# Kernel tuning notes

Hardware: AMD Instinct MI355X
Metric: run time of the kernel (lower is better)

The kernel has to match this reference:

```python
import jax, jax.numpy as jnp
import numpy as np
import math

D, DF, H, L, V, T_MAX = 768, 3072, 12, 4, 32000, 2048
HD = D // H
B, T = 2, 2048


def setup_inputs() -> dict:
    key = jax.random.key(0)
    ks = jax.random.split(key, 20)
    s = 0.02
    inp = {
        'ids': jax.random.randint(ks[0], (B, T), 0, V),
        'te': jax.random.normal(ks[1], (V, D), jnp.float32) * s,  # tied with head
        'pe': jax.random.normal(ks[2], (T_MAX, D), jnp.float32) * s,
        'ln1_s': jnp.ones((L, D), jnp.float32),
        'ln1_b': jnp.zeros((L, D), jnp.float32),
        'qkv_w': jax.random.normal(ks[3], (L, D, 3 * H * HD), jnp.float32) * s,
        'qkv_b': jnp.zeros((L, 3 * H * HD), jnp.float32),
        'out_w': jax.random.normal(ks[4], (L, H * HD, D), jnp.float32) * s,
        'out_b': jnp.zeros((L, D), jnp.float32),
        'ln2_s': jnp.ones((L, D), jnp.float32),
        'ln2_b': jnp.zeros((L, D), jnp.float32),
        'up_w': jax.random.normal(ks[5], (L, D, DF), jnp.float32) * s,
        'up_b': jnp.zeros((L, DF), jnp.float32),
        'dn_w': jax.random.normal(ks[6], (L, DF, D), jnp.float32) * s,
        'dn_b': jnp.zeros((L, D), jnp.float32),
        'lnf_s': jnp.ones((D,), jnp.float32),
        'lnf_b': jnp.zeros((D,), jnp.float32),
    }
    return inp


def _layernorm(x, s, b, eps=1e-5):
    mu = jnp.mean(x, axis=-1, keepdims=True)
    var = jnp.mean(jnp.square(x - mu), axis=-1, keepdims=True)
    return (x - mu) * jax.lax.rsqrt(var + eps) * s + b


def reference(ids, te, pe, ln1_s, ln1_b, qkv_w, qkv_b, out_w, out_b,
              ln2_s, ln2_b, up_w, up_b, dn_w, dn_b, lnf_s, lnf_b):
    b, t = ids.shape
    x = te[ids] + pe[jnp.arange(t)][None, :, :]  # [b,t,d]
    causal = jnp.tril(jnp.ones((t, t), bool))[None, None]  # [1,1,t,t]
    neg = jnp.asarray(-jnp.inf, x.dtype)
    for i in range(L):
        h = _layernorm(x, ln1_s[i], ln1_b[i])
        qkv = (h @ qkv_w[i] + qkv_b[i]).reshape(b, t, 3, H, HD)
        q, k, v = [jnp.moveaxis(qkv[:, :, j], 1, 2) for j in range(3)]  # [b,h,t,hd]
        sc = jnp.einsum('bhqd,bhkd->bhqk', q, k) / math.sqrt(HD)
        sc = jnp.where(causal, sc, neg)
        a = jax.nn.softmax(sc, axis=-1)
        o = jnp.einsum('bhqk,bhkd->bhqd', a, v)
        o = jnp.moveaxis(o, 1, 2).reshape(b, t, H * HD)
        x = x + o @ out_w[i] + out_b[i]
        h = _layernorm(x, ln2_s[i], ln2_b[i])
        x = x + jax.nn.silu(h @ up_w[i] + up_b[i]) @ dn_w[i] + dn_b[i]
    logits = _layernorm(x, lnf_s, lnf_b) @ te.T  # tied head, no bias
    return logits
```

## Files before the change

kernel.cpp:

```cpp
#include <hip/hip_runtime.h>

typedef unsigned short u16;

#define TSEQ 2048
#define DMODEL 768
#define DFF 3072
#define NHEAD 12
#define HDIM 64
#define NLAYER 4
#define NVOCAB 32000
#define MROWS 4096

typedef __attribute__((ext_vector_type(8))) __bf16 bf16x8;
typedef __attribute__((ext_vector_type(4))) float f32x4;
typedef __attribute__((ext_vector_type(8))) unsigned short us8;

__device__ __forceinline__ float u2f(u16 u) {
  return __uint_as_float(((unsigned int)u) << 16);
}
__device__ __forceinline__ u16 f2bu(float f) {
  unsigned int u = __float_as_uint(f);
  u += 0x7fffu + ((u >> 16) & 1u);
  return (u16)(u >> 16);
}
__device__ __forceinline__ int probe_f32(const void* probe) {
  return ((const u16*)probe)[0] == 0 ? 1 : 0;
}
__device__ __forceinline__ float ldf(const void* p, size_t i, int f32) {
  return f32 ? ((const float*)p)[i] : u2f(((const u16*)p)[i]);
}
__device__ __forceinline__ void ld8(const void* p, size_t i, int f32, float* o) {
  if (f32) {
    const float* q = (const float*)p + i;
    float4 a = *(const float4*)q, b = *(const float4*)(q + 4);
    o[0]=a.x; o[1]=a.y; o[2]=a.z; o[3]=a.w; o[4]=b.x; o[5]=b.y; o[6]=b.z; o[7]=b.w;
  } else {
    const u16* q = (const u16*)p + i;
    ushort4 a = *(const ushort4*)q, b = *(const ushort4*)(q + 4);
    o[0]=u2f(a.x); o[1]=u2f(a.y); o[2]=u2f(a.z); o[3]=u2f(a.w);
    o[4]=u2f(b.x); o[5]=u2f(b.y); o[6]=u2f(b.z); o[7]=u2f(b.w);
  }
}
__device__ __forceinline__ us8 pack8(const float* f) {
  us8 r;
#pragma unroll
  for (int i = 0; i < 8; i++) r[i] = f2bu(f[i]);
  return r;
}

__global__ __launch_bounds__(256) void embed_kernel(const int* __restrict__ ids,
    const void* __restrict__ te, const void* __restrict__ pe, float* __restrict__ x,
    const void* probe) {
  int f32 = probe_f32(probe);
  int m = blockIdx.x;
  int t = m & (TSEQ - 1);
  int id = ids[m];
  float* xr = x + (size_t)m * DMODEL;
  for (int d = threadIdx.x; d < DMODEL; d += 256)
    xr[d] = ldf(te, (size_t)id * DMODEL + d, f32) + ldf(pe, (size_t)t * DMODEL + d, f32);
}

__global__ __launch_bounds__(256) void ln_kernel(const float* __restrict__ x,
    const void* __restrict__ s, const void* __restrict__ b, long soff,
    float* __restrict__ h, const void* probe) {
  int f32 = probe_f32(probe);
  int m = blockIdx.x;
  const float* xr = x + (size_t)m * DMODEL;
  float v[3];
  float lsum = 0.f, lsq = 0.f;
#pragma unroll
  for (int j = 0; j < 3; j++) {
    float t = xr[threadIdx.x + j * 256];
    v[j] = t; lsum += t; lsq += t * t;
  }
#pragma unroll
  for (int off = 32; off > 0; off >>= 1) {
    lsum += __shfl_down(lsum, off);
    lsq  += __shfl_down(lsq, off);
  }
  __shared__ float wsum[4], wsq[4];
  __shared__ float mu_s, rs_s;
  int wid = threadIdx.x >> 6, lane = threadIdx.x & 63;
  if (lane == 0) { wsum[wid] = lsum; wsq[wid] = lsq; }
  __syncthreads();
  if (threadIdx.x == 0) {
    float su = wsum[0] + wsum[1] + wsum[2] + wsum[3];
    float sq = wsq[0] + wsq[1] + wsq[2] + wsq[3];
    float mu = su * (1.f / DMODEL);
    float var = sq * (1.f / DMODEL) - mu * mu;
    mu_s = mu;
    rs_s = rsqrtf(var + 1e-5f);
  }
  __syncthreads();
  float mu = mu_s, rs = rs_s;
  float* hr = h + (size_t)m * DMODEL;
#pragma unroll
  for (int j = 0; j < 3; j++) {
    int d = threadIdx.x + j * 256;
    hr[d] = (v[j] - mu) * rs * ldf(s, soff + d, f32) + ldf(b, soff + d, f32);
  }
}

__global__ __launch_bounds__(256) void wtrans_kernel(const void* __restrict__ W,
    u16* __restrict__ Wt, int K, int N, const void* probe) {
  const int f32 = probe_f32(probe);
  __shared__ u16 t[64][33];
  const size_t ls = (size_t)K * N;
  const size_t off = (size_t)blockIdx.z * ls;
  const int k0 = blockIdx.y << 6, n0 = blockIdx.x << 5;
  const int tid = threadIdx.x;
  const int tn = tid & 31, tk8 = tid >> 5;
#pragma unroll
  for (int p = 0; p < 8; p++) {
    int k = (p << 3) + tk8;
    t[k][tn] = f2bu(ldf(W, off + (size_t)(k0 + k) * N + n0 + tn, f32));
  }
  __syncthreads();
  const int kp = (tid & 31) << 1, nb = tid >> 5;
#pragma unroll
  for (int p = 0; p < 4; p++) {
    int n = (p << 3) + nb;
    ushort2 v; v.x = t[kp][n]; v.y = t[kp + 1][n];
    *(ushort2*)&Wt[off + (size_t)(n0 + n) * K + k0 + kp] = v;
  }
}

__global__ __launch_bounds__(256) void cvt_bf16_kernel(const void* __restrict__ src,
    u16* __restrict__ dst, size_t n, const void* probe) {
  const int f32 = probe_f32(probe);
  size_t i = ((size_t)blockIdx.x * 256 + threadIdx.x) * 8;
  if (i >= n) return;
  float v[8];
  ld8(src, i, f32, v);
  *(us8*)&dst[i] = pack8(v);
}

__global__ __launch_bounds__(256) void gemm_nn(const float* __restrict__ A,
    const void* __restrict__ W, long woff, const void* __restrict__ bias, long boff,
    const float* resid, float* C, int N, int K, int mode, const void* probe) {
  int f32 = probe_f32(probe);
  __shared__ float As[16][132];
  __shared__ float Bs[16][132];
  const int tid = threadIdx.x;
  const int m0 = blockIdx.y << 7, n0 = blockIdx.x << 7;
  const int rbase = (tid >> 4) << 3;
  const int cbase = (tid & 15) << 3;
  const int ar = tid >> 1, ak = (tid & 1) << 3;
  const int wk = tid >> 4, wc = (tid & 15) << 3;
  float acc[8][8];
#pragma unroll
  for (int i = 0; i < 8; i++)
#pragma unroll
    for (int j = 0; j < 8; j++) acc[i][j] = 0.f;

  const float* Ab = A + (size_t)(m0 + ar) * K + ak;
  for (int k0 = 0; k0 < K; k0 += 16) {
    float4 a0 = *(const float4*)(Ab + k0);
    float4 a1 = *(const float4*)(Ab + k0 + 4);
    As[ak + 0][ar] = a0.x; As[ak + 1][ar] = a0.y; As[ak + 2][ar] = a0.z; As[ak + 3][ar] = a0.w;
    As[ak + 4][ar] = a1.x; As[ak + 5][ar] = a1.y; As[ak + 6][ar] = a1.z; As[ak + 7][ar] = a1.w;
    float w[8];
    ld8(W, (size_t)woff + (size_t)(k0 + wk) * N + n0 + wc, f32, w);
    *(float4*)&Bs[wk][wc]     = make_float4(w[0], w[1], w[2], w[3]);
    *(float4*)&Bs[wk][wc + 4] = make_float4(w[4], w[5], w[6], w[7]);
    __syncthreads();
#pragma unroll
    for (int kk = 0; kk < 16; kk++) {
      float a[8], b[8];
      *(float4*)&a[0] = *(const float4*)&As[kk][rbase];
      *(float4*)&a[4] = *(const float4*)&As[kk][rbase + 4];
      *(float4*)&b[0] = *(const float4*)&Bs[kk][cbase];
      *(float4*)&b[4] = *(const float4*)&Bs[kk][cbase + 4];
#pragma unroll
      for (int i = 0; i < 8; i++)
#pragma unroll
        for (int j = 0; j < 8; j++)
          acc[i][j] = fmaf(a[i], b[j], acc[i][j]);
    }
    __syncthreads();
  }
  float bv[8];
#pragma unroll
  for (int j = 0; j < 8; j++) bv[j] = ldf(bias, boff + n0 + cbase + j, f32);
#pragma unroll
  for (int i = 0; i < 8; i++) {
    size_t off = (size_t)(m0 + rbase + i) * N + n0 + cbase;
    float v[8];
#pragma unroll
    for (int j = 0; j < 8; j++) v[j] = acc[i][j] + bv[j];
    if (mode == 1) {
      float4 r0 = *(const float4*)(resid + off);
      float4 r1 = *(const float4*)(resid + off + 4);
      v[0] += r0.x; v[1] += r0.y; v[2] += r0.z; v[3] += r0.w;
      v[4] += r1.x; v[5] += r1.y; v[6] += r1.z; v[7] += r1.w;
    } else if (mode == 2) {
#pragma unroll
      for (int j = 0; j < 8; j++) v[j] = v[j] / (1.f + __expf(-v[j]));
    }
    *(float4*)(C + off)     = make_float4(v[0], v[1], v[2], v[3]);
    *(float4*)(C + off + 4) = make_float4(v[4], v[5], v[6], v[7]);
  }
}

__global__ __launch_bounds__(256) void gemm_mfma(const float* __restrict__ A,
    const u16* __restrict__ Wt, long woff, const void* __restrict__ bias, long boff,
    const float* resid, float* C, int N, int K, int mode, const void* probe) {
  const int f32 = probe_f32(probe);
  __shared__ __align__(16) u16 As[128][40];
  __shared__ __align__(16) u16 Bs[128][40];
  const int tid = threadIdx.x;
  const int m0 = blockIdx.y << 7, n0 = blockIdx.x << 7;
  const int lane = tid & 63;
  const int wr = ((tid >> 7) & 1) << 6;
  const int wc = ((tid >> 6) & 1) << 6;
  const int fm = lane & 15;
  const int kl = lane >> 4;
  const int sr = tid >> 1, sc = (tid & 1) << 4;

  f32x4 acc[4][4];
#pragma unroll
  for (int i = 0; i < 4; i++)
#pragma unroll
    for (int j = 0; j < 4; j++) acc[i][j] = (f32x4){0.f, 0.f, 0.f, 0.f};

  const float* Ab = A + (size_t)(m0 + sr) * K + sc;
  const u16* Wb = Wt + (size_t)woff + (size_t)(n0 + sr) * K + sc;

  for (int k0 = 0; k0 < K; k0 += 32) {
    float av[16];
    *(float4*)&av[0]  = *(const float4*)(Ab + k0);
    *(float4*)&av[4]  = *(const float4*)(Ab + k0 + 4);
    *(float4*)&av[8]  = *(const float4*)(Ab + k0 + 8);
    *(float4*)&av[12] = *(const float4*)(Ab + k0 + 12);
    us8 w0 = *(const us8*)(Wb + k0);
    us8 w1 = *(const us8*)(Wb + k0 + 8);
    *(us8*)&As[sr][sc]     = pack8(av);
    *(us8*)&As[sr][sc + 8] = pack8(av + 8);
    *(us8*)&Bs[sr][sc]     = w0;
    *(us8*)&Bs[sr][sc + 8] = w1;
    __syncthreads();
    bf16x8 af[4], bfr[4];
#pragma unroll
    for (int i = 0; i < 4; i++)
      af[i] = *reinterpret_cast<const bf16x8*>(&As[wr + i * 16 + fm][kl << 3]);
#pragma unroll
    for (int j = 0; j < 4; j++)
      bfr[j] = *reinterpret_cast<const bf16x8*>(&Bs[wc + j * 16 + fm][kl << 3]);
#pragma unroll
    for (int i = 0; i < 4; i++)
#pragma unroll
      for (int j = 0; j < 4; j++)
        acc[i][j] = __builtin_amdgcn_mfma_f32_16x16x32_bf16(af[i], bfr[j], acc[i][j], 0, 0, 0);
    __syncthreads();
  }

  const int rb = m0 + wr + (kl << 2);
  const int cb = n0 + wc + fm;
  float bv[4];
#pragma unroll
  for (int j = 0; j < 4; j++) bv[j] = ldf(bias, boff + cb + j * 16, f32);
#pragma unroll
  for (int i = 0; i < 4; i++) {
#pragma unroll
    for (int e = 0; e < 4; e++) {
      size_t roff = (size_t)(rb + i * 16 + e) * N;
#pragma unroll
      for (int j = 0; j < 4; j++) {
        float v = acc[i][j][e] + bv[j];
        if (mode == 1) v += resid[roff + cb + j * 16];
        else if (mode == 2) v = v / (1.f + __expf(-v));
        C[roff + cb + j * 16] = v;
      }
    }
  }
}

__global__ __launch_bounds__(256) void gemm_head_mfma(const float* __restrict__ A,
    const u16* __restrict__ Wtb, const void* __restrict__ Wt, void* __restrict__ C,
    const void* probe) {
  const int f32 = probe_f32(probe);
  __shared__ __align__(16) u16 As[128][40];
  __shared__ __align__(16) u16 Bs[128][40];
  const int tid = threadIdx.x;
  const int m0 = blockIdx.x << 7, n0 = blockIdx.y << 7;
  const int lane = tid & 63;
  const int wr = ((tid >> 7) & 1) << 6;
  const int wc = ((tid >> 6) & 1) << 6;
  const int fm = lane & 15;
  const int kl = lane >> 4;
  const int sr = tid >> 1, sc = (tid & 1) << 4;

  f32x4 acc[4][4];
#pragma unroll
  for (int i = 0; i < 4; i++)
#pragma unroll
    for (int j = 0; j < 4; j++) acc[i][j] = (f32x4){0.f, 0.f, 0.f, 0.f};

  const float* Ab = A + (size_t)(m0 + sr) * DMODEL + sc;
  const size_t wbase = (size_t)(n0 + sr) * DMODEL + sc;
  const u16* Wbb = Wtb ? Wtb + wbase : nullptr;

  for (int k0 = 0; k0 < DMODEL; k0 += 32) {
    float av[16];
    *(float4*)&av[0]  = *(const float4*)(Ab + k0);
    *(float4*)&av[4]  = *(const float4*)(Ab + k0 + 4);
    *(float4*)&av[8]  = *(const float4*)(Ab + k0 + 8);
    *(float4*)&av[12] = *(const float4*)(Ab + k0 + 12);
    *(us8*)&As[sr][sc]     = pack8(av);
    *(us8*)&As[sr][sc + 8] = pack8(av + 8);
    if (Wbb) {
      *(us8*)&Bs[sr][sc]     = *(const us8*)(Wbb + k0);
      *(us8*)&Bs[sr][sc + 8] = *(const us8*)(Wbb + k0 + 8);
    } else {
      float wv[16];
      ld8(Wt, wbase + k0, f32, wv);
      ld8(Wt, wbase + k0 + 8, f32, wv + 8);
      *(us8*)&Bs[sr][sc]     = pack8(wv);
      *(us8*)&Bs[sr][sc + 8] = pack8(wv + 8);
    }
    __syncthreads();
    bf16x8 af[4], bfr[4];
#pragma unroll
    for (int i = 0; i < 4; i++)
      af[i] = *reinterpret_cast<const bf16x8*>(&As[wr + i * 16 + fm][kl << 3]);
#pragma unroll
    for (int j = 0; j < 4; j++)
      bfr[j] = *reinterpret_cast<const bf16x8*>(&Bs[wc + j * 16 + fm][kl << 3]);
#pragma unroll
    for (int i = 0; i < 4; i++)
#pragma unroll
      for (int j = 0; j < 4; j++)
        acc[i][j] = __builtin_amdgcn_mfma_f32_16x16x32_bf16(af[i], bfr[j], acc[i][j], 0, 0, 0);
    __syncthreads();
  }

  const int rbase = m0 + wr + (kl << 2);
  const int cbase = n0 + wc + fm;
#pragma unroll
  for (int i = 0; i < 4; i++) {
#pragma unroll
    for (int j = 0; j < 4; j++) {
#pragma unroll
      for (int e = 0; e < 4; e++) {
        size_t off = (size_t)(rbase + i * 16 + e) * NVOCAB + cbase + j * 16;
        if (f32) ((float*)C)[off] = acc[i][j][e];
        else     ((u16*)C)[off]   = f2bu(acc[i][j][e]);
      }
    }
  }
}

__global__ __launch_bounds__(256) void attn_mfma(const float* __restrict__ qkv,
                                                 float* __restrict__ o) {
  const int qt = blockIdx.x, hh = blockIdx.y, bb = blockIdx.z;
  __shared__ __align__(16) u16 Ks[64][72];
  __shared__ __align__(16) u16 Vt[64][72];
  __shared__ __align__(16) u16 Ps[64][72];
  const int tid = threadIdx.x;
  const int w = tid >> 6, lane = tid & 63;
  const int fm = lane & 15, kl = lane >> 4;

  bf16x8 aq[2];
  {
    const float* qrow = qkv + ((size_t)(bb * TSEQ + qt * 64 + w * 16 + fm)) * 2304 + hh * 64;
#pragma unroll
    for (int c = 0; c < 2; c++) {
      float4 q0 = *(const float4*)(qrow + c * 32 + kl * 8);
      float4 q1 = *(const float4*)(qrow + c * 32 + kl * 8 + 4);
      float qv[8] = {q0.x * 0.125f, q0.y * 0.125f, q0.z * 0.125f, q0.w * 0.125f,
                     q1.x * 0.125f, q1.y * 0.125f, q1.z * 0.125f, q1.w * 0.125f};
      us8 u = pack8(qv);
      aq[c] = *(bf16x8*)&u;
    }
  }

  float m_r[4], l_r[4];
#pragma unroll
  for (int e = 0; e < 4; e++) { m_r[e] = -3e38f; l_r[e] = 0.f; }
  f32x4 oacc[4];
#pragma unroll
  for (int j = 0; j < 4; j++) oacc[j] = (f32x4){0.f, 0.f, 0.f, 0.f};

  for (int kt = 0; kt <= qt; kt++) {
    const size_t kbase = ((size_t)(bb * TSEQ + kt * 64)) * 2304 + hh * 64;
#pragma unroll
    for (int it = 0; it < 2; it++) {
      int idx = tid + it * 256;
      int row = idx >> 3, cb = (idx & 7) << 3;
      const float* kr = qkv + kbase + (size_t)row * 2304 + 768 + cb;
      float4 k0 = *(const float4*)kr, k1 = *(const float4*)(kr + 4);
      float kv[8] = {k0.x, k0.y, k0.z, k0.w, k1.x, k1.y, k1.z, k1.w};
      *(us8*)&Ks[row][cb] = pack8(kv);
      int row2 = idx & 63, cb2 = (idx >> 6) << 3;
      const float* vr = qkv + kbase + (size_t)row2 * 2304 + 1536 + cb2;
      float4 v0 = *(const float4*)vr, v1 = *(const float4*)(vr + 4);
      float vv[8] = {v0.x, v0.y, v0.z, v0.w, v1.x, v1.y, v1.z, v1.w};
#pragma unroll
      for (int e = 0; e < 8; e++) Vt[cb2 + e][row2] = f2bu(vv[e]);
    }
    __syncthreads();

    f32x4 sacc[4];
#pragma unroll
    for (int j = 0; j < 4; j++) sacc[j] = (f32x4){0.f, 0.f, 0.f, 0.f};
#pragma unroll
    for (int ck = 0; ck < 2; ck++) {
      bf16x8 kb[4];
#pragma unroll
      for (int j = 0; j < 4; j++)
        kb[j] = *reinterpret_cast<const bf16x8*>(&Ks[j * 16 + fm][ck * 32 + (kl << 3)]);
#pragma unroll
      for (int j = 0; j < 4; j++)
        sacc[j] = __builtin_amdgcn_mfma_f32_16x16x32_bf16(aq[ck], kb[j], sacc[j], 0, 0, 0);
    }
    if (kt == qt) {
      const int qrow0 = w * 16 + (kl << 2);
#pragma unroll
      for (int j = 0; j < 4; j++)
#pragma unroll
        for (int e = 0; e < 4; e++)
          if (j * 16 + fm > qrow0 + e) sacc[j][e] = -3e38f;
    }
    float pmax[4];
#pragma unroll
    for (int e = 0; e < 4; e++) {
      pmax[e] = fmaxf(fmaxf(sacc[0][e], sacc[1][e]), fmaxf(sacc[2][e], sacc[3][e]));
    }
#pragma unroll
    for (int msk = 1; msk < 16; msk <<= 1)
#pragma unroll
      for (int e = 0; e < 4; e++) pmax[e] = fmaxf(pmax[e], __shfl_xor(pmax[e], msk));
    float al[4];
#pragma unroll
    for (int e = 0; e < 4; e++) {
      float nm = fmaxf(m_r[e], pmax[e]);
      al[e] = __expf(m_r[e] - nm);
      m_r[e] = nm;
    }
    float psum[4] = {0.f, 0.f, 0.f, 0.f};
#pragma unroll
    for (int j = 0; j < 4; j++)
#pragma unroll
      for (int e = 0; e < 4; e++) {
        float p = __expf(sacc[j][e] - m_r[e]);
        sacc[j][e] = p;
        psum[e] += p;
      }
#pragma unroll
    for (int j = 0; j < 4; j++)
#pragma unroll
      for (int e = 0; e < 4; e++)
        Ps[w * 16 + (kl << 2) + e][j * 16 + fm] = f2bu(sacc[j][e]);
#pragma unroll
    for (int msk = 1; msk < 16; msk <<= 1)
#pragma unroll
      for (int e = 0; e < 4; e++) psum[e] += __shfl_xor(psum[e], msk);
#pragma unroll
    for (int e = 0; e < 4; e++) l_r[e] = l_r[e] * al[e] + psum[e];
#pragma unroll
    for (int j = 0; j < 4; j++)
#pragma unroll
      for (int e = 0; e < 4; e++) oacc[j][e] *= al[e];
#pragma unroll
    for (int ck = 0; ck < 2; ck++) {
      bf16x8 pa = *reinterpret_cast<const bf16x8*>(&Ps[w * 16 + fm][ck * 32 + (kl << 3)]);
      bf16x8 vb[4];
#pragma unroll
      for (int j = 0; j < 4; j++)
        vb[j] = *reinterpret_cast<const bf16x8*>(&Vt[j * 16 + fm][ck * 32 + (kl << 3)]);
#pragma unroll
      for (int j = 0; j < 4; j++)
        oacc[j] = __builtin_amdgcn_mfma_f32_16x16x32_bf16(pa, vb[j], oacc[j], 0, 0, 0);
    }
    __syncthreads();
  }

  float linv[4];
#pragma unroll
  for (int e = 0; e < 4; e++) linv[e] = 1.f / l_r[e];
#pragma unroll
  for (int e = 0; e < 4; e++) {
    size_t ob = ((size_t)(bb * TSEQ + qt * 64 + w * 16 + (kl << 2) + e)) * DMODEL + hh * 64 + fm;
#pragma unroll
    for (int j = 0; j < 4; j++) o[ob + j * 16] = oacc[j][e] * linv[e];
  }
}

extern "C" void kernel_launch(void* const* d_in, const int* in_sizes, int n_in,
                              void* d_out, int out_size, void* d_ws, size_t ws_size,
                              hipStream_t stream) {
  const int* ids = (const int*)d_in[0];
  const void* te    = d_in[1];
  const void* pe    = d_in[2];
  const void* ln1_s = d_in[3];
  const void* ln1_b = d_in[4];
  const void* qkv_w = d_in[5];
  const void* qkv_b = d_in[6];
  const void* out_w = d_in[7];
  const void* out_b = d_in[8];
  const void* ln2_s = d_in[9];
  const void* ln2_b = d_in[10];
  const void* up_w  = d_in[11];
  const void* up_b  = d_in[12];
  const void* dn_w  = d_in[13];
  const void* dn_b  = d_in[14];
  const void* lnf_s = d_in[15];
  const void* lnf_b = d_in[16];
  const void* probe = ln1_s;

  float* x  = (float*)d_ws;
  float* h  = x + (size_t)MROWS * DMODEL;
  float* ob = h + (size_t)MROWS * DMODEL;
  float* qu = ob + (size_t)MROWS * DMODEL;

  const size_t base_f = (size_t)MROWS * DMODEL * 3 + (size_t)MROWS * DFF;
  u16* wt = (u16*)(x + base_f);
  const size_t qkv_t_sz = (size_t)2304 * 768;
  const size_t out_t_sz = (size_t)768 * 768;
  const size_t up_t_sz  = (size_t)3072 * 768;
  const size_t dn_t_sz  = (size_t)768 * 3072;
  u16* qkv_t = wt;
  u16* out_t = qkv_t + NLAYER * qkv_t_sz;
  u16* up_t  = out_t + NLAYER * out_t_sz;
  u16* dn_t  = up_t  + NLAYER * up_t_sz;
  const size_t w_sz = NLAYER * (qkv_t_sz + out_t_sz + up_t_sz + dn_t_sz);
  u16* tebf  = dn_t + NLAYER * dn_t_sz;
  const size_t te_sz = (size_t)NVOCAB * DMODEL;
  const size_t need_basic = base_f * 4 + w_sz * 2;
  const size_t need_te    = need_basic + te_sz * 2;
  const int fast = ws_size >= need_basic;
  const u16* head_wt = nullptr;
  int cvt_te = 0;
  if (ws_size >= need_te) { head_wt = tebf; cvt_te = 1; }

  embed_kernel<<<MROWS, 256, 0, stream>>>(ids, te, pe, x, probe);

  if (fast) {
    wtrans_kernel<<<dim3(2304/32, 768/64, NLAYER), 256, 0, stream>>>(qkv_w, qkv_t, 768, 2304, probe);
    wtrans_kernel<<<dim3(768/32,  768/64, NLAYER), 256, 0, stream>>>(out_w, out_t, 768, 768, probe);
    wtrans_kernel<<<dim3(3072/32, 768/64, NLAYER), 256, 0, stream>>>(up_w,  up_t,  768, 3072, probe);
    wtrans_kernel<<<dim3(768/32, 3072/64, NLAYER), 256, 0, stream>>>(dn_w,  dn_t,  3072, 768, probe);
  }
  if (cvt_te)
    cvt_bf16_kernel<<<(int)((te_sz / 8 + 255) / 256), 256, 0, stream>>>(te, tebf, te_sz, probe);

  for (int l = 0; l < NLAYER; l++) {
    long lD = (long)l * DMODEL;
    ln_kernel<<<MROWS, 256, 0, stream>>>(x, ln1_s, ln1_b, lD, h, probe);
    if (fast)
      gemm_mfma<<<dim3(18, 32), 256, 0, stream>>>(h, qkv_t, (long)l * qkv_t_sz,
          qkv_b, (long)l * 2304, nullptr, qu, 2304, DMODEL, 0, probe);
    else
      gemm_nn<<<dim3(18, 32), 256, 0, stream>>>(h, qkv_w, (long)l * DMODEL * 2304,
          qkv_b, (long)l * 2304, nullptr, qu, 2304, DMODEL, 0, probe);
    attn_mfma<<<dim3(32, 12, 2), 256, 0, stream>>>(qu, ob);
    if (fast)
      gemm_mfma<<<dim3(6, 32), 256, 0, stream>>>(ob, out_t, (long)l * out_t_sz,
          out_b, lD, x, x, DMODEL, DMODEL, 1, probe);
    else
      gemm_nn<<<dim3(6, 32), 256, 0, stream>>>(ob, out_w, (long)l * DMODEL * DMODEL,
          out_b, lD, x, x, DMODEL, DMODEL, 1, probe);
    ln_kernel<<<MROWS, 256, 0, stream>>>(x, ln2_s, ln2_b, lD, h, probe);
    if (fast)
      gemm_mfma<<<dim3(24, 32), 256, 0, stream>>>(h, up_t, (long)l * up_t_sz,
          up_b, (long)l * DFF, nullptr, qu, DFF, DMODEL, 2, probe);
    else
      gemm_nn<<<dim3(24, 32), 256, 0, stream>>>(h, up_w, (long)l * DMODEL * DFF,
          up_b, (long)l * DFF, nullptr, qu, DFF, DMODEL, 2, probe);
    if (fast)
      gemm_mfma<<<dim3(6, 32), 256, 0, stream>>>(qu, dn_t, (long)l * dn_t_sz,
          dn_b, lD, x, x, DMODEL, DFF, 1, probe);
    else
      gemm_nn<<<dim3(6, 32), 256, 0, stream>>>(qu, dn_w, (long)l * DFF * DMODEL,
          dn_b, lD, x, x, DMODEL, DFF, 1, probe);
  }
  ln_kernel<<<MROWS, 256, 0, stream>>>(x, lnf_s, lnf_b, 0, h, probe);
  gemm_head_mfma<<<dim3(32, 250), 256, 0, stream>>>(h, head_wt, te, d_out, probe);
}
```

Baseline: 2.669 ms.

## Store intermediate activations in bf16 and drop fp32 fallback GEMM paths

LayerNorm output, QKV, attention output and MLP hidden activations are now written as bf16 instead of fp32. The MFMA GEMMs, attention and head kernels load bf16 directly instead of loading fp32 and packing. This halves activation memory traffic and removes conversion work across several kernels. The workspace-size checks and the scalar fp32 gemm_nn fallback are removed, so the code now assumes the workspace is always large enough. The 1/sqrt(d) scale moves from Q to the score accumulators, and rounding changes slightly because bf16 rounding now happens at the producer.

New measurement: 2.360 ms. -11.6%, faster.

```diff
diff --git a/kernel.cpp b/kernel.cpp
--- a/kernel.cpp
+++ b/kernel.cpp
@@ -62,7 +62,7 @@
 
 __global__ __launch_bounds__(256) void ln_kernel(const float* __restrict__ x,
     const void* __restrict__ s, const void* __restrict__ b, long soff,
-    float* __restrict__ h, const void* probe) {
+    u16* __restrict__ h, const void* probe) {
   int f32 = probe_f32(probe);
   int m = blockIdx.x;
   const float* xr = x + (size_t)m * DMODEL;
@@ -93,11 +93,11 @@
   }
   __syncthreads();
   float mu = mu_s, rs = rs_s;
-  float* hr = h + (size_t)m * DMODEL;
+  u16* hr = h + (size_t)m * DMODEL;
 #pragma unroll
   for (int j = 0; j < 3; j++) {
     int d = threadIdx.x + j * 256;
-    hr[d] = (v[j] - mu) * rs * ldf(s, soff + d, f32) + ldf(b, soff + d, f32);
+    hr[d] = f2bu((v[j] - mu) * rs * ldf(s, soff + d, f32) + ldf(b, soff + d, f32));
   }
 }
 
@@ -135,76 +135,9 @@
   *(us8*)&dst[i] = pack8(v);
 }
 
-__global__ __launch_bounds__(256) void gemm_nn(const float* __restrict__ A,
-    const void* __restrict__ W, long woff, const void* __restrict__ bias, long boff,
-    const float* resid, float* C, int N, int K, int mode, const void* probe) {
-  int f32 = probe_f32(probe);
-  __shared__ float As[16][132];
-  __shared__ float Bs[16][132];
-  const int tid = threadIdx.x;
-  const int m0 = blockIdx.y << 7, n0 = blockIdx.x << 7;
-  const int rbase = (tid >> 4) << 3;
-  const int cbase = (tid & 15) << 3;
-  const int ar = tid >> 1, ak = (tid & 1) << 3;
-  const int wk = tid >> 4, wc = (tid & 15) << 3;
-  float acc[8][8];
-#pragma unroll
-  for (int i = 0; i < 8; i++)
-#pragma unroll
-    for (int j = 0; j < 8; j++) acc[i][j] = 0.f;
-
-  const float* Ab = A + (size_t)(m0 + ar) * K + ak;
-  for (int k0 = 0; k0 < K; k0 += 16) {
-    float4 a0 = *(const float4*)(Ab + k0);
-    float4 a1 = *(const float4*)(Ab + k0 + 4);
-    As[ak + 0][ar] = a0.x; As[ak + 1][ar] = a0.y; As[ak + 2][ar] = a0.z; As[ak + 3][ar] = a0.w;
-    As[ak + 4][ar] = a1.x; As[ak + 5][ar] = a1.y; As[ak + 6][ar] = a1.z; As[ak + 7][ar] = a1.w;
-    float w[8];
-    ld8(W, (size_t)woff + (size_t)(k0 + wk) * N + n0 + wc, f32, w);
-    *(float4*)&Bs[wk][wc]     = make_float4(w[0], w[1], w[2], w[3]);
-    *(float4*)&Bs[wk][wc + 4] = make_float4(w[4], w[5], w[6], w[7]);
-    __syncthreads();
-#pragma unroll
-    for (int kk = 0; kk < 16; kk++) {
-      float a[8], b[8];
-      *(float4*)&a[0] = *(const float4*)&As[kk][rbase];
-      *(float4*)&a[4] = *(const float4*)&As[kk][rbase + 4];
-      *(float4*)&b[0] = *(const float4*)&Bs[kk][cbase];
-      *(float4*)&b[4] = *(const float4*)&Bs[kk][cbase + 4];
-#pragma unroll
-      for (int i = 0; i < 8; i++)
-#pragma unroll
-        for (int j = 0; j < 8; j++)
-          acc[i][j] = fmaf(a[i], b[j], acc[i][j]);
-    }
-    __syncthreads();
-  }
-  float bv[8];
-#pragma unroll
-  for (int j = 0; j < 8; j++) bv[j] = ldf(bias, boff + n0 + cbase + j, f32);
-#pragma unroll
-  for (int i = 0; i < 8; i++) {
-    size_t off = (size_t)(m0 + rbase + i) * N + n0 + cbase;
-    float v[8];
-#pragma unroll
-    for (int j = 0; j < 8; j++) v[j] = acc[i][j] + bv[j];
-    if (mode == 1) {
-      float4 r0 = *(const float4*)(resid + off);
-      float4 r1 = *(const float4*)(resid + off + 4);
-      v[0] += r0.x; v[1] += r0.y; v[2] += r0.z; v[3] += r0.w;
-      v[4] += r1.x; v[5] += r1.y; v[6] += r1.z; v[7] += r1.w;
-    } else if (mode == 2) {
-#pragma unroll
-      for (int j = 0; j < 8; j++) v[j] = v[j] / (1.f + __expf(-v[j]));
-    }
-    *(float4*)(C + off)     = make_float4(v[0], v[1], v[2], v[3]);
-    *(float4*)(C + off + 4) = make_float4(v[4], v[5], v[6], v[7]);
-  }
-}
-
-__global__ __launch_bounds__(256) void gemm_mfma(const float* __restrict__ A,
+__global__ __launch_bounds__(256) void gemm_mfma(const u16* __restrict__ A,
     const u16* __restrict__ Wt, long woff, const void* __restrict__ bias, long boff,
-    const float* resid, float* C, int N, int K, int mode, const void* probe) {
+    const float* resid, void* C, int N, int K, int mode, const void* probe) {
   const int f32 = probe_f32(probe);
   __shared__ __align__(16) u16 As[128][40];
   __shared__ __align__(16) u16 Bs[128][40];
@@ -223,19 +156,16 @@
 #pragma unroll
     for (int j = 0; j < 4; j++) acc[i][j] = (f32x4){0.f, 0.f, 0.f, 0.f};
 
-  const float* Ab = A + (size_t)(m0 + sr) * K + sc;
+  const u16* Ab = A + (size_t)(m0 + sr) * K + sc;
   const u16* Wb = Wt + (size_t)woff + (size_t)(n0 + sr) * K + sc;
 
   for (int k0 = 0; k0 < K; k0 += 32) {
-    float av[16];
-    *(float4*)&av[0]  = *(const float4*)(Ab + k0);
-    *(float4*)&av[4]  = *(const float4*)(Ab + k0 + 4);
-    *(float4*)&av[8]  = *(const float4*)(Ab + k0 + 8);
-    *(float4*)&av[12] = *(const float4*)(Ab + k0 + 12);
+    us8 a0 = *(const us8*)(Ab + k0);
+    us8 a1 = *(const us8*)(Ab + k0 + 8);
     us8 w0 = *(const us8*)(Wb + k0);
     us8 w1 = *(const us8*)(Wb + k0 + 8);
-    *(us8*)&As[sr][sc]     = pack8(av);
-    *(us8*)&As[sr][sc + 8] = pack8(av + 8);
+    *(us8*)&As[sr][sc]     = a0;
+    *(us8*)&As[sr][sc + 8] = a1;
     *(us8*)&Bs[sr][sc]     = w0;
     *(us8*)&Bs[sr][sc + 8] = w1;
     __syncthreads();
@@ -267,17 +197,19 @@
 #pragma unroll
       for (int j = 0; j < 4; j++) {
         float v = acc[i][j][e] + bv[j];
-        if (mode == 1) v += resid[roff + cb + j * 16];
-        else if (mode == 2) v = v / (1.f + __expf(-v));
-        C[roff + cb + j * 16] = v;
+        if (mode == 1) {
+          ((float*)C)[roff + cb + j * 16] = v + resid[roff + cb + j * 16];
+        } else {
+          if (mode == 2) v = v / (1.f + __expf(-v));
+          ((u16*)C)[roff + cb + j * 16] = f2bu(v);
+        }
       }
     }
   }
 }
 
-__global__ __launch_bounds__(256) void gemm_head_mfma(const float* __restrict__ A,
-    const u16* __restrict__ Wtb, const void* __restrict__ Wt, void* __restrict__ C,
-    const void* probe) {
+__global__ __launch_bounds__(256) void gemm_head_mfma(const u16* __restrict__ A,
+    const u16* __restrict__ Wtb, void* __restrict__ C, const void* probe) {
   const int f32 = probe_f32(probe);
   __shared__ __align__(16) u16 As[128][40];
   __shared__ __align__(16) u16 Bs[128][40];
@@ -296,28 +228,18 @@
 #pragma unroll
     for (int j = 0; j < 4; j++) acc[i][j] = (f32x4){0.f, 0.f, 0.f, 0.f};
 
-  const float* Ab = A + (size_t)(m0 + sr) * DMODEL + sc;
-  const size_t wbase = (size_t)(n0 + sr) * DMODEL + sc;
-  const u16* Wbb = Wtb ? Wtb + wbase : nullptr;
+  const u16* Ab = A + (size_t)(m0 + sr) * DMODEL + sc;
+  const u16* Wb = Wtb + (size_t)(n0 + sr) * DMODEL + sc;
 
   for (int k0 = 0; k0 < DMODEL; k0 += 32) {
-    float av[16];
-    *(float4*)&av[0]  = *(const float4*)(Ab + k0);
-    *(float4*)&av[4]  = *(const float4*)(Ab + k0 + 4);
-    *(float4*)&av[8]  = *(const float4*)(Ab + k0 + 8);
-    *(float4*)&av[12] = *(const float4*)(Ab + k0 + 12);
-    *(us8*)&As[sr][sc]     = pack8(av);
-    *(us8*)&As[sr][sc + 8] = pack8(av + 8);
-    if (Wbb) {
-      *(us8*)&Bs[sr][sc]     = *(const us8*)(Wbb + k0);
-      *(us8*)&Bs[sr][sc + 8] = *(const us8*)(Wbb + k0 + 8);
-    } else {
-      float wv[16];
-      ld8(Wt, wbase + k0, f32, wv);
-      ld8(Wt, wbase + k0 + 8, f32, wv + 8);
-      *(us8*)&Bs[sr][sc]     = pack8(wv);
-      *(us8*)&Bs[sr][sc + 8] = pack8(wv + 8);
-    }
+    us8 a0 = *(const us8*)(Ab + k0);
+    us8 a1 = *(const us8*)(Ab + k0 + 8);
+    us8 w0 = *(const us8*)(Wb + k0);
+    us8 w1 = *(const us8*)(Wb + k0 + 8);
+    *(us8*)&As[sr][sc]     = a0;
+    *(us8*)&As[sr][sc + 8] = a1;
+    *(us8*)&Bs[sr][sc]     = w0;
+    *(us8*)&Bs[sr][sc + 8] = w1;
     __syncthreads();
     bf16x8 af[4], bfr[4];
 #pragma unroll
@@ -350,8 +272,8 @@
   }
 }
 
-__global__ __launch_bounds__(256) void attn_mfma(const float* __restrict__ qkv,
-                                                 float* __restrict__ o) {
+__global__ __launch_bounds__(256) void attn_mfma(const u16* __restrict__ qkv,
+                                                 u16* __restrict__ o) {
   const int qt = blockIdx.x, hh = blockIdx.y, bb = blockIdx.z;
   __shared__ __align__(16) u16 Ks[64][72];
   __shared__ __align__(16) u16 Vt[64][72];
@@ -362,14 +284,10 @@
 
   bf16x8 aq[2];
   {
-    const float* qrow = qkv + ((size_t)(bb * TSEQ + qt * 64 + w * 16 + fm)) * 2304 + hh * 64;
+    const u16* qrow = qkv + ((size_t)(bb * TSEQ + qt * 64 + w * 16 + fm)) * 2304 + hh * 64;
 #pragma unroll
     for (int c = 0; c < 2; c++) {
-      float4 q0 = *(const float4*)(qrow + c * 32 + kl * 8);
-      float4 q1 = *(const float4*)(qrow + c * 32 + kl * 8 + 4);
-      float qv[8] = {q0.x * 0.125f, q0.y * 0.125f, q0.z * 0.125f, q0.w * 0.125f,
-                     q1.x * 0.125f, q1.y * 0.125f, q1.z * 0.125f, q1.w * 0.125f};
-      us8 u = pack8(qv);
+      us8 u = *(const us8*)(qrow + c * 32 + kl * 8);
       aq[c] = *(bf16x8*)&u;
     }
   }
@@ -387,16 +305,11 @@
     for (int it = 0; it < 2; it++) {
       int idx = tid + it * 256;
       int row = idx >> 3, cb = (idx & 7) << 3;
-      const float* kr = qkv + kbase + (size_t)row * 2304 + 768 + cb;
-      float4 k0 = *(const float4*)kr, k1 = *(const float4*)(kr + 4);
-      float kv[8] = {k0.x, k0.y, k0.z, k0.w, k1.x, k1.y, k1.z, k1.w};
-      *(us8*)&Ks[row][cb] = pack8(kv);
+      *(us8*)&Ks[row][cb] = *(const us8*)(qkv + kbase + (size_t)row * 2304 + 768 + cb);
       int row2 = idx & 63, cb2 = (idx >> 6) << 3;
-      const float* vr = qkv + kbase + (size_t)row2 * 2304 + 1536 + cb2;
-      float4 v0 = *(const float4*)vr, v1 = *(const float4*)(vr + 4);
-      float vv[8] = {v0.x, v0.y, v0.z, v0.w, v1.x, v1.y, v1.z, v1.w};
-#pragma unroll
-      for (int e = 0; e < 8; e++) Vt[cb2 + e][row2] = f2bu(vv[e]);
+      us8 vv = *(const us8*)(qkv + kbase + (size_t)row2 * 2304 + 1536 + cb2);
+#pragma unroll
+      for (int e = 0; e < 8; e++) Vt[cb2 + e][row2] = vv[e];
     }
     __syncthreads();
 
@@ -413,6 +326,10 @@
       for (int j = 0; j < 4; j++)
         sacc[j] = __builtin_amdgcn_mfma_f32_16x16x32_bf16(aq[ck], kb[j], sacc[j], 0, 0, 0);
     }
+#pragma unroll
+    for (int j = 0; j < 4; j++)
+#pragma unroll
+      for (int e = 0; e < 4; e++) sacc[j][e] *= 0.125f;
     if (kt == qt) {
       const int qrow0 = w * 16 + (kl << 2);
 #pragma unroll
@@ -482,7 +399,7 @@
   for (int e = 0; e < 4; e++) {
     size_t ob = ((size_t)(bb * TSEQ + qt * 64 + w * 16 + (kl << 2) + e)) * DMODEL + hh * 64 + fm;
 #pragma unroll
-    for (int j = 0; j < 4; j++) o[ob + j * 16] = oacc[j][e] * linv[e];
+    for (int j = 0; j < 4; j++) o[ob + j * 16] = f2bu(oacc[j][e] * linv[e]);
   }
 }
 
@@ -509,12 +426,10 @@
   const void* probe = ln1_s;
 
   float* x  = (float*)d_ws;
-  float* h  = x + (size_t)MROWS * DMODEL;
-  float* ob = h + (size_t)MROWS * DMODEL;
-  float* qu = ob + (size_t)MROWS * DMODEL;
-
-  const size_t base_f = (size_t)MROWS * DMODEL * 3 + (size_t)MROWS * DFF;
-  u16* wt = (u16*)(x + base_f);
+  u16* h    = (u16*)(x + (size_t)MROWS * DMODEL);
+  u16* ob   = h + (size_t)MROWS * DMODEL;
+  u16* qu   = ob + (size_t)MROWS * DMODEL;
+  u16* wt   = qu + (size_t)MROWS * DFF;
   const size_t qkv_t_sz = (size_t)2304 * 768;
   const size_t out_t_sz = (size_t)768 * 768;
   const size_t up_t_sz  = (size_t)3072 * 768;
@@ -523,57 +438,31 @@
   u16* out_t = qkv_t + NLAYER * qkv_t_sz;
   u16* up_t  = out_t + NLAYER * out_t_sz;
   u16* dn_t  = up_t  + NLAYER * up_t_sz;
-  const size_t w_sz = NLAYER * (qkv_t_sz + out_t_sz + up_t_sz + dn_t_sz);
   u16* tebf  = dn_t + NLAYER * dn_t_sz;
   const size_t te_sz = (size_t)NVOCAB * DMODEL;
-  const size_t need_basic = base_f * 4 + w_sz * 2;
-  const size_t need_te    = need_basic + te_sz * 2;
-  const int fast = ws_size >= need_basic;
-  const u16* head_wt = nullptr;
-  int cvt_te = 0;
-  if (ws_size >= need_te) { head_wt = tebf; cvt_te = 1; }
 
   embed_kernel<<<MROWS, 256, 0, stream>>>(ids, te, pe, x, probe);
 
-  if (fast) {
-    wtrans_kernel<<<dim3(2304/32, 768/64, NLAYER), 256, 0, stream>>>(qkv_w, qkv_t, 768, 2304, probe);
-    wtrans_kernel<<<dim3(768/32,  768/64, NLAYER), 256, 0, stream>>>(out_w, out_t, 768, 768, probe);
-    wtrans_kernel<<<dim3(3072/32, 768/64, NLAYER), 256, 0, stream>>>(up_w,  up_t,  768, 3072, probe);
-    wtrans_kernel<<<dim3(768/32, 3072/64, NLAYER), 256, 0, stream>>>(dn_w,  dn_t,  3072, 768, probe);
-  }
-  if (cvt_te)
-    cvt_bf16_kernel<<<(int)((te_sz / 8 + 255) / 256), 256, 0, stream>>>(te, tebf, te_sz, probe);
+  wtrans_kernel<<<dim3(2304/32, 768/64, NLAYER), 256, 0, stream>>>(qkv_w, qkv_t, 768, 2304, probe);
+  wtrans_kernel<<<dim3(768/32,  768/64, NLAYER), 256, 0, stream>>>(out_w, out_t, 768, 768, probe);
+  wtrans_kernel<<<dim3(3072/32, 768/64, NLAYER), 256, 0, stream>>>(up_w,  up_t,  768, 3072, probe);
+  wtrans_kernel<<<dim3(768/32, 3072/64, NLAYER), 256, 0, stream>>>(dn_w,  dn_t,  3072, 768, probe);
+  cvt_bf16_kernel<<<(int)((te_sz / 8 + 255) / 256), 256, 0, stream>>>(te, tebf, te_sz, probe);
 
   for (int l = 0; l < NLAYER; l++) {
     long lD = (long)l * DMODEL;
     ln_kernel<<<MROWS, 256, 0, stream>>>(x, ln1_s, ln1_b, lD, h, probe);
-    if (fast)
-      gemm_mfma<<<dim3(18, 32), 256, 0, stream>>>(h, qkv_t, (long)l * qkv_t_sz,
-          qkv_b, (long)l * 2304, nullptr, qu, 2304, DMODEL, 0, probe);
-    else
-      gemm_nn<<<dim3(18, 32), 256, 0, stream>>>(h, qkv_w, (long)l * DMODEL * 2304,
-          qkv_b, (long)l * 2304, nullptr, qu, 2304, DMODEL, 0, probe);
+    gemm_mfma<<<dim3(18, 32), 256, 0, stream>>>(h, qkv_t, (long)l * qkv_t_sz,
+        qkv_b, (long)l * 2304, nullptr, qu, 2304, DMODEL, 0, probe);
     attn_mfma<<<dim3(32, 12, 2), 256, 0, stream>>>(qu, ob);
-    if (fast)
-      gemm_mfma<<<dim3(6, 32), 256, 0, stream>>>(ob, out_t, (long)l * out_t_sz,
-          out_b, lD, x, x, DMODEL, DMODEL, 1, probe);
-    else
-      gemm_nn<<<dim3(6, 32), 256, 0, stream>>>(ob, out_w, (long)l * DMODEL * DMODEL,
-          out_b, lD, x, x, DMODEL, DMODEL, 1, probe);
+    gemm_mfma<<<dim3(6, 32), 256, 0, stream>>>(ob, out_t, (long)l * out_t_sz,
+        out_b, lD, x, x, DMODEL, DMODEL, 1, probe);
     ln_kernel<<<MROWS, 256, 0, stream>>>(x, ln2_s, ln2_b, lD, h, probe);
-    if (fast)
-      gemm_mfma<<<dim3(24, 32), 256, 0, stream>>>(h, up_t, (long)l * up_t_sz,
-          up_b, (long)l * DFF, nullptr, qu, DFF, DMODEL, 2, probe);
-    else
-      gemm_nn<<<dim3(24, 32), 256, 0, stream>>>(h, up_w, (long)l * DMODEL * DFF,
-          up_b, (long)l * DFF, nullptr, qu, DFF, DMODEL, 2, probe);
-    if (fast)
-      gemm_mfma<<<dim3(6, 32), 256, 0, stream>>>(qu, dn_t, (long)l * dn_t_sz,
-          dn_b, lD, x, x, DMODEL, DFF, 1, probe);
-    else
-      gemm_nn<<<dim3(6, 32), 256, 0, stream>>>(qu, dn_w, (long)l * DFF * DMODEL,
-          dn_b, lD, x, x, DMODEL, DFF, 1, probe);
+    gemm_mfma<<<dim3(24, 32), 256, 0, stream>>>(h, up_t, (long)l * up_t_sz,
+        up_b, (long)l * DFF, nullptr, qu, DFF, DMODEL, 2, probe);
+    gemm_mfma<<<dim3(6, 32), 256, 0, stream>>>(qu, dn_t, (long)l * dn_t_sz,
+        dn_b, lD, x, x, DMODEL, DFF, 1, probe);
   }
   ln_kernel<<<MROWS, 256, 0, stream>>>(x, lnf_s, lnf_b, 0, h, probe);
-  gemm_head_mfma<<<dim3(32, 250), 256, 0, stream>>>(h, head_wt, te, d_out, probe);
-}
+  gemm_head_mfma<<<dim3(32, 250), 256, 0, stream>>>(h, tebf, d_out, probe);
+}
```
